# Kernel tuning notes

Measured on AMD Instinct MI355X. Metric: run time of the kernel, lower is better.

Reference implementation:

```python
import jax, jax.numpy as jnp
import numpy as np
from jax.scipy.stats import norm

N_TOK, D_MODEL, N_EXP, N_SEL = 16384, 4096, 16, 4
NOISE_EPS = 0.01
LOSS_LAMBDA = 0.01


def setup_inputs() -> dict:
    key = jax.random.key(0)
    kx, k1, k2, kn, kz = jax.random.split(key, 5)
    x = jax.random.normal(kx, (N_TOK, D_MODEL), dtype=jnp.float32)
    w1 = jax.random.normal(k1, (N_EXP, D_MODEL), dtype=jnp.float32) * 0.02
    w2 = jax.random.normal(k2, (N_EXP, N_EXP), dtype=jnp.float32) * 0.02
    wn = jax.random.normal(kn, (N_EXP, D_MODEL), dtype=jnp.float32) * 0.02
    noise = jax.random.normal(kz, (N_TOK, N_EXP), dtype=jnp.float32)
    return {"x": x, "w1": w1, "w2": w2, "wn": wn, "noise": noise}


def _cv_squared(v, eps=1e-10):
    # torch .var() is unbiased (ddof=1)
    return jnp.var(v, ddof=1) / (jnp.mean(v) ** 2 + eps)


def reference(x, w1, w2, wn, noise):
    # MLP gate: Linear(D->E, no bias) -> tanh -> Linear(E->E, no bias)
    logits_gate = jnp.einsum("te,fe->tf", jnp.tanh(jnp.einsum("td,ed->te", x, w1)), w2)
    noise_control = jax.nn.softplus(jnp.einsum("td,ed->te", x, wn)) + NOISE_EPS
    logits_noise = noise * noise_control
    logits = logits_gate + logits_noise  # [T, E]

    m = min(N_SEL + 1, N_EXP)  # k+1 values for threshold computation
    top_logits, top_indices = jax.lax.top_k(logits, m)  # [T, m]
    top_k_logits = top_logits[:, :N_SEL]
    top_k_indices = top_indices[:, :N_SEL]
    top_k_scores = jax.nn.softmax(top_k_logits, axis=1)  # [T, k]

    # importance: scatter top-k scores back to dense [T, E]
    rows = jnp.arange(N_TOK)[:, None]
    scores_filtered = jnp.zeros_like(logits).at[rows, top_k_indices].set(top_k_scores)
    importance = scores_filtered.sum(0)  # [E]

    # load: smooth estimator via Normal CDF (faithful to source, which
    # compares logits_noise against the in/out thresholds)
    threshold_if_in = top_logits[:, N_SEL:N_SEL + 1]       # (k+1)-th top value, [T,1]
    threshold_if_out = top_logits[:, N_SEL - 1:N_SEL]      # k-th top value, [T,1]
    is_in = logits_noise > threshold_if_in
    prob_if_in = norm.cdf((logits_gate - threshold_if_in) / noise_control)
    prob_if_out = norm.cdf((logits_gate - threshold_if_out) / noise_control)
    prob = jnp.where(is_in, prob_if_in, prob_if_out)
    load = prob.sum(0)  # [E]

    gate_loss = LOSS_LAMBDA * (_cv_squared(importance) + _cv_squared(load))
    return top_k_indices, top_k_scores, gate_loss
```

## Files before the change

kernel.cpp:

```cpp
#include <hip/hip_runtime.h>
#include <math.h>

#define N_TOK   16384
#define D_MODEL 4096
#define N_EXP   16
#define N_SEL   4
#define WELEM   (N_EXP * D_MODEL)
#define TILES   2

typedef __bf16 bf16x8 __attribute__((ext_vector_type(8)));
typedef float  f32x4  __attribute__((ext_vector_type(4)));

#define MFMA(a, b, c) __builtin_amdgcn_mfma_f32_16x16x32_bf16((a), (b), (c), 0, 0, 0)

__global__ __launch_bounds__(256) void wprep_kernel(const float* __restrict__ w1,
                                                    const float* __restrict__ wn,
                                                    __bf16* __restrict__ wbuf,
                                                    float* __restrict__ g_acc)
{
    const int i = blockIdx.x * 256 + threadIdx.x;
    if (blockIdx.x == 0 && threadIdx.x < 2 * N_EXP) g_acc[threadIdx.x] = 0.f;
    {
        const float v = w1[i];
        const __bf16 h = (__bf16)v;  const float r1 = v - (float)h;
        const __bf16 m = (__bf16)r1; const float r2 = r1 - (float)m;
        wbuf[i] = h; wbuf[WELEM + i] = m; wbuf[2 * WELEM + i] = (__bf16)r2;
    }
    {
        const float v = wn[i];
        const __bf16 h = (__bf16)v;  const float r1 = v - (float)h;
        const __bf16 m = (__bf16)r1; const float r2 = r1 - (float)m;
        wbuf[3 * WELEM + i] = h; wbuf[4 * WELEM + i] = m; wbuf[5 * WELEM + i] = (__bf16)r2;
    }
}

__device__ __forceinline__ void split8(const float4 a, const float4 b,
                                       bf16x8& h, bf16x8& m, bf16x8& l)
{
    const float v[8] = {a.x, a.y, a.z, a.w, b.x, b.y, b.z, b.w};
    #pragma unroll
    for (int j = 0; j < 8; ++j) {
        const float vv = v[j];
        const __bf16 hh = (__bf16)vv;  const float r1 = vv - (float)hh;
        const __bf16 mm = (__bf16)r1;  const float r2 = r1 - (float)mm;
        h[j] = hh; m[j] = mm; l[j] = (__bf16)r2;
    }
}

__global__ __launch_bounds__(512, 4) void gate_kernel(
    const float* __restrict__ x, const __bf16* __restrict__ wbuf,
    const float* __restrict__ w2, const float* __restrict__ noise,
    float* __restrict__ out, float* __restrict__ g_imp, float* __restrict__ g_load)
{
    __shared__ float smem[2][8 * 32 * 33];
    __shared__ float s_imp[N_EXP], s_ld[N_EXP];

    const int tid  = threadIdx.x;
    const int lane = tid & 63;
    const int wv   = tid >> 6;
    const int ml   = lane & 15;
    const int q    = lane >> 4;
    const int t0   = blockIdx.x * (TILES * 16);

    const __bf16* w1h = wbuf;
    const __bf16* w1m = wbuf + WELEM;
    const __bf16* w1l = wbuf + 2 * WELEM;
    const __bf16* wnh = wbuf + 3 * WELEM;
    const __bf16* wnm = wbuf + 4 * WELEM;
    const __bf16* wnl = wbuf + 5 * WELEM;

    const int woff = ml * D_MODEL + wv * 512 + q * 8;

    int gb0, gb1, gb2, gb3, lb0, lb1, lb2, lb3;
    {
#define MAP(P, GB, LB)                                           \
        {   const int fid  = (P) * 512 + tid;                    \
            const int slot = fid & 7;                            \
            const int s    = fid >> 3;                           \
            const int r    = s >> 5;                             \
            const int t    = s & 31;                             \
            GB = (t0 + t) * D_MODEL + r * 512 + slot * 4;        \
            LB = (r * 32 + t) * 33 + slot * 4;  }
        MAP(0, gb0, lb0) MAP(1, gb1, lb1) MAP(2, gb2, lb2) MAP(3, gb3, lb3)
#undef MAP
    }
    const int lr0 = (wv * 32 + ml) * 33 + q * 8;
    const int lr1 = lr0 + 16 * 33;

    f32x4 c1[TILES], c2[TILES];
    #pragma unroll
    for (int tt = 0; tt < TILES; ++tt) {
        c1[tt] = (f32x4){0.f, 0.f, 0.f, 0.f};
        c2[tt] = (f32x4){0.f, 0.f, 0.f, 0.f};
    }

    float* bufA = smem[0];
    float* bufB = smem[1];

    {
        const float4 s0 = *(const float4*)(x + gb0);
        const float4 s1 = *(const float4*)(x + gb1);
        const float4 s2 = *(const float4*)(x + gb2);
        const float4 s3 = *(const float4*)(x + gb3);
        *(float4*)(bufA + lb0) = s0;
        *(float4*)(bufA + lb1) = s1;
        *(float4*)(bufA + lb2) = s2;
        *(float4*)(bufA + lb3) = s3;
        __syncthreads();
    }

#define STEP(CUR, NXT, IT)                                                    \
    {                                                                          \
        const int ko = (IT) * 32;                                              \
        const bf16x8 a1h = *(const bf16x8*)(w1h + woff + ko);                  \
        const bf16x8 a1m = *(const bf16x8*)(w1m + woff + ko);                  \
        const bf16x8 a1l = *(const bf16x8*)(w1l + woff + ko);                  \
        const bf16x8 a2h = *(const bf16x8*)(wnh + woff + ko);                  \
        const bf16x8 a2m = *(const bf16x8*)(wnm + woff + ko);                  \
        const bf16x8 a2l = *(const bf16x8*)(wnl + woff + ko);                  \
        float4 sg0, sg1, sg2, sg3;                                             \
        if ((IT) < 15) {                                                       \
            const int co = ((IT) + 1) * 32;                                    \
            sg0 = *(const float4*)(x + gb0 + co);                              \
            sg1 = *(const float4*)(x + gb1 + co);                              \
            sg2 = *(const float4*)(x + gb2 + co);                              \
            sg3 = *(const float4*)(x + gb3 + co);                              \
        }                                                                      \
        const float4 xa0 = *(const float4*)((CUR) + lr0);                      \
        const float4 xb0 = *(const float4*)((CUR) + lr0 + 4);                  \
        const float4 xa1 = *(const float4*)((CUR) + lr1);                      \
        const float4 xb1 = *(const float4*)((CUR) + lr1 + 4);                  \
        bf16x8 xh0, xm0, xl0, xh1, xm1, xl1;                                   \
        split8(xa0, xb0, xh0, xm0, xl0);                                       \
        split8(xa1, xb1, xh1, xm1, xl1);                                       \
        c1[0] = MFMA(a1h, xh0, c1[0]);  c2[0] = MFMA(a2h, xh0, c2[0]);         \
        c1[1] = MFMA(a1h, xh1, c1[1]);  c2[1] = MFMA(a2h, xh1, c2[1]);         \
        c1[0] = MFMA(a1h, xm0, c1[0]);  c2[0] = MFMA(a2h, xm0, c2[0]);         \
        c1[1] = MFMA(a1h, xm1, c1[1]);  c2[1] = MFMA(a2h, xm1, c2[1]);         \
        c1[0] = MFMA(a1m, xh0, c1[0]);  c2[0] = MFMA(a2m, xh0, c2[0]);         \
        c1[1] = MFMA(a1m, xh1, c1[1]);  c2[1] = MFMA(a2m, xh1, c2[1]);         \
        c1[0] = MFMA(a1h, xl0, c1[0]);  c2[0] = MFMA(a2h, xl0, c2[0]);         \
        c1[1] = MFMA(a1h, xl1, c1[1]);  c2[1] = MFMA(a2h, xl1, c2[1]);         \
        c1[0] = MFMA(a1l, xh0, c1[0]);  c2[0] = MFMA(a2l, xh0, c2[0]);         \
        c1[1] = MFMA(a1l, xh1, c1[1]);  c2[1] = MFMA(a2l, xh1, c2[1]);         \
        c1[0] = MFMA(a1m, xm0, c1[0]);  c2[0] = MFMA(a2m, xm0, c2[0]);         \
        c1[1] = MFMA(a1m, xm1, c1[1]);  c2[1] = MFMA(a2m, xm1, c2[1]);         \
        if ((IT) < 15) {                                                       \
            *(float4*)((NXT) + lb0) = sg0;                                     \
            *(float4*)((NXT) + lb1) = sg1;                                     \
            *(float4*)((NXT) + lb2) = sg2;                                     \
            *(float4*)((NXT) + lb3) = sg3;                                     \
        }                                                                      \
        __syncthreads();                                                       \
    }

    #pragma unroll
    for (int ith = 0; ith < 8; ++ith) {
        STEP(bufA, bufB, 2 * ith)
        STEP(bufB, bufA, 2 * ith + 1)
    }
#undef STEP

    float* red  = smem[0];
    float* dsum = smem[1];

    #pragma unroll
    for (int tt = 0; tt < TILES; ++tt) {
        #pragma unroll
        for (int r = 0; r < 4; ++r) {
            red[((wv * TILES + tt) * 16 + ml) * 33 + q * 4 + r]      = c1[tt][r];
            red[((wv * TILES + tt) * 16 + ml) * 33 + 16 + q * 4 + r] = c2[tt][r];
        }
    }
    __syncthreads();

    for (int idx = tid; idx < TILES * 512; idx += 512) {
        const int tt = idx >> 9, tk = (idx >> 5) & 15, o = idx & 31;
        float s = 0.f;
        #pragma unroll
        for (int w = 0; w < 8; ++w) s += red[((w * TILES + tt) * 16 + tk) * 33 + o];
        dsum[(tt * 16 + tk) * 33 + o] = s;
    }
    if (tid < N_EXP) { s_imp[tid] = 0.f; s_ld[tid] = 0.f; }
    __syncthreads();

    if (tid < TILES * 16) {
        const int tt = tid >> 4, tk = tid & 15;
        const int t = t0 + tid;
        float dot[32];
        #pragma unroll
        for (int e = 0; e < 32; ++e) dot[e] = dsum[(tt * 16 + tk) * 33 + e];

        float th[N_EXP], nc[N_EXP];
        #pragma unroll
        for (int e = 0; e < N_EXP; ++e) th[e] = tanhf(dot[e]);
        #pragma unroll
        for (int e = 0; e < N_EXP; ++e) {
            const float v = dot[N_EXP + e];
            nc[e] = fmaxf(v, 0.f) + log1pf(expf(-fabsf(v))) + 0.01f;
        }

        float lg[N_EXP];
        #pragma unroll
        for (int f = 0; f < N_EXP; ++f) {
            float s = 0.f;
            #pragma unroll
            for (int e = 0; e < N_EXP; ++e) s = fmaf(th[e], w2[f * 16 + e], s);
            lg[f] = s;
        }

        float ln[N_EXP], v[N_EXP];
        {
            const float4* nz = (const float4*)(noise + (size_t)t * 16);
            const float4 n0 = nz[0], n1 = nz[1], n2 = nz[2], n3 = nz[3];
            const float nzv[16] = {n0.x, n0.y, n0.z, n0.w, n1.x, n1.y, n1.z, n1.w,
                                   n2.x, n2.y, n2.z, n2.w, n3.x, n3.y, n3.z, n3.w};
            #pragma unroll
            for (int e = 0; e < N_EXP; ++e) {
                ln[e] = nzv[e] * nc[e];
                v[e]  = lg[e] + ln[e];
            }
        }

        float tv[5]; int ti[5];
        #pragma unroll
        for (int j = 0; j < 5; ++j) {
            float best = -INFINITY; int bi = 0;
            #pragma unroll
            for (int e = 0; e < N_EXP; ++e) {
                bool taken = false;
                #pragma unroll
                for (int jj = 0; jj < 5; ++jj)
                    if (jj < j) taken = taken || (ti[jj] == e);
                if (!taken && v[e] > best) { best = v[e]; bi = e; }
            }
            tv[j] = best; ti[j] = bi;
        }

        const float mx = tv[0];
        float ex[4], ssum = 0.f;
        #pragma unroll
        for (int j = 0; j < 4; ++j) { ex[j] = expf(tv[j] - mx); ssum += ex[j]; }
        const float inv = 1.f / ssum;
        float sc[4];
        #pragma unroll
        for (int j = 0; j < 4; ++j) sc[j] = ex[j] * inv;

        #pragma unroll
        for (int j = 0; j < 4; ++j) atomicAdd(&s_imp[ti[j]], sc[j]);

        const float thr_in = tv[4], thr_out = tv[3];
        #pragma unroll
        for (int e = 0; e < N_EXP; ++e) {
            const bool  is_in = ln[e] > thr_in;
            const float thr   = is_in ? thr_in : thr_out;
            const float z     = (lg[e] - thr) / nc[e];
            const float prob  = 0.5f * (1.f + erff(z * 0.70710678118654752f));
            atomicAdd(&s_ld[e], prob);
        }

        ((float4*)out)[t] = make_float4((float)ti[0], (float)ti[1],
                                        (float)ti[2], (float)ti[3]);
        ((float4*)(out + N_TOK * N_SEL))[t] = make_float4(sc[0], sc[1], sc[2], sc[3]);
    }
    __syncthreads();
    if (tid < N_EXP)            atomicAdd(&g_imp[tid], s_imp[tid]);
    else if (tid < 2 * N_EXP)   atomicAdd(&g_load[tid - N_EXP], s_ld[tid - N_EXP]);
}

__global__ void loss_kernel(const float* __restrict__ g_imp,
                            const float* __restrict__ g_load,
                            float* __restrict__ out)
{
    if (threadIdx.x == 0 && blockIdx.x == 0) {
        double mi = 0.0, ml = 0.0;
        for (int e = 0; e < N_EXP; ++e) { mi += g_imp[e]; ml += g_load[e]; }
        mi /= N_EXP; ml /= N_EXP;
        double vi = 0.0, vl = 0.0;
        for (int e = 0; e < N_EXP; ++e) {
            const double di = g_imp[e] - mi;  vi += di * di;
            const double dl = g_load[e] - ml; vl += dl * dl;
        }
        vi /= (N_EXP - 1); vl /= (N_EXP - 1);
        const double ci = vi / (mi * mi + 1e-10);
        const double cl = vl / (ml * ml + 1e-10);
        out[N_TOK * N_SEL * 2] = (float)(0.01 * (ci + cl));
    }
}

extern "C" void kernel_launch(void* const* d_in, const int* in_sizes, int n_in,
                              void* d_out, int out_size, void* d_ws, size_t ws_size,
                              hipStream_t stream)
{
    const float* x     = (const float*)d_in[0];
    const float* w1    = (const float*)d_in[1];
    const float* w2    = (const float*)d_in[2];
    const float* wn    = (const float*)d_in[3];
    const float* noise = (const float*)d_in[4];
    float* out = (float*)d_out;

    __bf16* wbuf  = (__bf16*)d_ws;
    float*  g_imp = (float*)((char*)d_ws + (1 << 20));
    float*  g_load = g_imp + N_EXP;

    wprep_kernel<<<WELEM / 256, 256, 0, stream>>>(w1, wn, wbuf, g_imp);
    gate_kernel<<<N_TOK / (TILES * 16), 512, 0, stream>>>(x, wbuf, w2, noise, out,
                                                          g_imp, g_load);
    loss_kernel<<<1, 64, 0, stream>>>(g_imp, g_load, out);
}
```

Baseline: 405.7 us.

## Stage contiguous 256-float windows of x per token instead of strided chunks

Changes the x staging so each pipeline step loads a contiguous 256-float window per token (64 threads per row), rather than eight 32-float pieces spread 512 floats apart. Each wave now takes a different 32-element slice within the window, and the weight fragment offsets are remapped to match. The intent is more contiguous global reads per token row, better coalescing and DRAM locality. The LDS row stride is padded to 260 to limit bank conflicts, and the reduction buffers move to fixed offsets in the flat shared array.

```diff
diff --git a/kernel.cpp b/kernel.cpp
--- a/kernel.cpp
+++ b/kernel.cpp
@@ -7,6 +7,10 @@
 #define N_SEL   4
 #define WELEM   (N_EXP * D_MODEL)
 #define TILES   2
+#define NWIN    16
+#define WINF    256
+#define TSTR    260
+#define BUFW    (32 * TSTR)
 
 typedef __bf16 bf16x8 __attribute__((ext_vector_type(8)));
 typedef float  f32x4  __attribute__((ext_vector_type(4)));
@@ -52,7 +56,7 @@
     const float* __restrict__ w2, const float* __restrict__ noise,
     float* __restrict__ out, float* __restrict__ g_imp, float* __restrict__ g_load)
 {
-    __shared__ float smem[2][8 * 32 * 33];
+    __shared__ float smem[2 * BUFW];
     __shared__ float s_imp[N_EXP], s_ld[N_EXP];
 
     const int tid  = threadIdx.x;
@@ -69,23 +73,21 @@
     const __bf16* wnm = wbuf + 4 * WELEM;
     const __bf16* wnl = wbuf + 5 * WELEM;
 
-    const int woff = ml * D_MODEL + wv * 512 + q * 8;
-
-    int gb0, gb1, gb2, gb3, lb0, lb1, lb2, lb3;
+    const int wofc = ml * D_MODEL + wv * 32 + q * 8;
+
+    int gi0, gi1, gi2, gi3, li0, li1, li2, li3;
     {
-#define MAP(P, GB, LB)                                           \
-        {   const int fid  = (P) * 512 + tid;                    \
-            const int slot = fid & 7;                            \
-            const int s    = fid >> 3;                           \
-            const int r    = s >> 5;                             \
-            const int t    = s & 31;                             \
-            GB = (t0 + t) * D_MODEL + r * 512 + slot * 4;        \
-            LB = (r * 32 + t) * 33 + slot * 4;  }
-        MAP(0, gb0, lb0) MAP(1, gb1, lb1) MAP(2, gb2, lb2) MAP(3, gb3, lb3)
+#define MAP(P, GI, LI)                                        \
+        {   const int fid = (P) * 512 + tid;                  \
+            const int tk  = fid >> 6;                         \
+            const int sl  = fid & 63;                         \
+            GI = (t0 + tk) * D_MODEL + sl * 4;                \
+            LI = tk * TSTR + sl * 4;  }
+        MAP(0, gi0, li0) MAP(1, gi1, li1) MAP(2, gi2, li2) MAP(3, gi3, li3)
 #undef MAP
     }
-    const int lr0 = (wv * 32 + ml) * 33 + q * 8;
-    const int lr1 = lr0 + 16 * 33;
+    const int lr0 = ml * TSTR + wv * 32 + q * 8;
+    const int lr1 = (16 + ml) * TSTR + wv * 32 + q * 8;
 
     f32x4 c1[TILES], c2[TILES];
     #pragma unroll
@@ -94,38 +96,38 @@
         c2[tt] = (f32x4){0.f, 0.f, 0.f, 0.f};
     }
 
-    float* bufA = smem[0];
-    float* bufB = smem[1];
+    float* bufA = smem;
+    float* bufB = smem + BUFW;
 
     {
-        const float4 s0 = *(const float4*)(x + gb0);
-        const float4 s1 = *(const float4*)(x + gb1);
-        const float4 s2 = *(const float4*)(x + gb2);
-        const float4 s3 = *(const float4*)(x + gb3);
-        *(float4*)(bufA + lb0) = s0;
-        *(float4*)(bufA + lb1) = s1;
-        *(float4*)(bufA + lb2) = s2;
-        *(float4*)(bufA + lb3) = s3;
+        const float4 s0 = *(const float4*)(x + gi0);
+        const float4 s1 = *(const float4*)(x + gi1);
+        const float4 s2 = *(const float4*)(x + gi2);
+        const float4 s3 = *(const float4*)(x + gi3);
+        *(float4*)(bufA + li0) = s0;
+        *(float4*)(bufA + li1) = s1;
+        *(float4*)(bufA + li2) = s2;
+        *(float4*)(bufA + li3) = s3;
         __syncthreads();
     }
 
-#define STEP(CUR, NXT, IT)                                                    \
+#define STEP(CUR, NXT, C)                                                     \
     {                                                                          \
-        const int ko = (IT) * 32;                                              \
-        const bf16x8 a1h = *(const bf16x8*)(w1h + woff + ko);                  \
-        const bf16x8 a1m = *(const bf16x8*)(w1m + woff + ko);                  \
-        const bf16x8 a1l = *(const bf16x8*)(w1l + woff + ko);                  \
-        const bf16x8 a2h = *(const bf16x8*)(wnh + woff + ko);                  \
-        const bf16x8 a2m = *(const bf16x8*)(wnm + woff + ko);                  \
-        const bf16x8 a2l = *(const bf16x8*)(wnl + woff + ko);                  \
         float4 sg0, sg1, sg2, sg3;                                             \
-        if ((IT) < 15) {                                                       \
-            const int co = ((IT) + 1) * 32;                                    \
-            sg0 = *(const float4*)(x + gb0 + co);                              \
-            sg1 = *(const float4*)(x + gb1 + co);                              \
-            sg2 = *(const float4*)(x + gb2 + co);                              \
-            sg3 = *(const float4*)(x + gb3 + co);                              \
+        if ((C) < NWIN - 1) {                                                  \
+            const int co = ((C) + 1) * WINF;                                   \
+            sg0 = *(const float4*)(x + gi0 + co);                              \
+            sg1 = *(const float4*)(x + gi1 + co);                              \
+            sg2 = *(const float4*)(x + gi2 + co);                              \
+            sg3 = *(const float4*)(x + gi3 + co);                              \
         }                                                                      \
+        const int wo = wofc + (C) * WINF;                                      \
+        const bf16x8 a1h = *(const bf16x8*)(w1h + wo);                         \
+        const bf16x8 a1m = *(const bf16x8*)(w1m + wo);                         \
+        const bf16x8 a1l = *(const bf16x8*)(w1l + wo);                         \
+        const bf16x8 a2h = *(const bf16x8*)(wnh + wo);                         \
+        const bf16x8 a2m = *(const bf16x8*)(wnm + wo);                         \
+        const bf16x8 a2l = *(const bf16x8*)(wnl + wo);                         \
         const float4 xa0 = *(const float4*)((CUR) + lr0);                      \
         const float4 xb0 = *(const float4*)((CUR) + lr0 + 4);                  \
         const float4 xa1 = *(const float4*)((CUR) + lr1);                      \
@@ -145,24 +147,24 @@
         c1[1] = MFMA(a1l, xh1, c1[1]);  c2[1] = MFMA(a2l, xh1, c2[1]);         \
         c1[0] = MFMA(a1m, xm0, c1[0]);  c2[0] = MFMA(a2m, xm0, c2[0]);         \
         c1[1] = MFMA(a1m, xm1, c1[1]);  c2[1] = MFMA(a2m, xm1, c2[1]);         \
-        if ((IT) < 15) {                                                       \
-            *(float4*)((NXT) + lb0) = sg0;                                     \
-            *(float4*)((NXT) + lb1) = sg1;                                     \
-            *(float4*)((NXT) + lb2) = sg2;                                     \
-            *(float4*)((NXT) + lb3) = sg3;                                     \
+        if ((C) < NWIN - 1) {                                                  \
+            *(float4*)((NXT) + li0) = sg0;                                     \
+            *(float4*)((NXT) + li1) = sg1;                                     \
+            *(float4*)((NXT) + li2) = sg2;                                     \
+            *(float4*)((NXT) + li3) = sg3;                                     \
         }                                                                      \
         __syncthreads();                                                       \
     }
 
     #pragma unroll
-    for (int ith = 0; ith < 8; ++ith) {
-        STEP(bufA, bufB, 2 * ith)
-        STEP(bufB, bufA, 2 * ith + 1)
+    for (int h = 0; h < NWIN / 2; ++h) {
+        STEP(bufA, bufB, 2 * h)
+        STEP(bufB, bufA, 2 * h + 1)
     }
 #undef STEP
 
-    float* red  = smem[0];
-    float* dsum = smem[1];
+    float* red  = smem;
+    float* dsum = smem + 8448;
 
     #pragma unroll
     for (int tt = 0; tt < TILES; ++tt) {
```

Result: no change. 401.2 us (-1.1%).
